# Optimization experiments

Hardware: AMD Instinct MI355X
Metric: run time of the kernel (lower is better)

The kernel has to match this reference:

```python
import jax, jax.numpy as jnp
import numpy as np

EPS = 1e-5  # torch InstanceNorm1d default eps
H = 64      # band_features


def instance_norm(x):
    # x: [B, T, F]; torch applies InstanceNorm1d on [B, F, T], i.e. normalize
    # over the length axis T per (batch, channel). No affine params.
    mu = jnp.mean(x, axis=1, keepdims=True)
    var = jnp.var(x, axis=1, keepdims=True)  # biased variance, as torch
    return (x - mu) * jax.lax.rsqrt(var + EPS)


def lstm_layer(x, Wih, Whh, bih, bhh):
    # x: [B, T, D_in]; Wih: [4H, D_in]; Whh: [4H, H]; gate order i,f,g,o (torch)
    B, T, _ = x.shape
    xp = jnp.einsum('btd,gd->btg', x, Wih) + bih + bhh   # [B, T, 4H]
    xp = jnp.swapaxes(xp, 0, 1)                          # [T, B, 4H]

    def step(carry, xt):
        h, c = carry
        gates = xt + h @ Whh.T                           # [B, 4H]
        i, f, g, o = jnp.split(gates, 4, axis=-1)
        c = jax.nn.sigmoid(f) * c + jax.nn.sigmoid(i) * jnp.tanh(g)
        h = jax.nn.sigmoid(o) * jnp.tanh(c)
        return (h, c), h

    h0 = jnp.zeros((B, H), x.dtype)
    _, hs = jax.lax.scan(step, (h0, h0), xp)             # hs: [T, B, H]
    return jnp.swapaxes(hs, 0, 1)                        # [B, T, H]


def setup_inputs() -> dict:
    key = jax.random.key(0)
    ks = jax.random.split(key, 12)
    B, T = 64, 4096
    bound = 1.0 / np.sqrt(H)  # torch LSTM/Linear default init scale

    def u(k, shape):
        return jax.random.uniform(k, shape, jnp.float32, -bound, bound)

    return {
        'x': jax.random.normal(ks[0], (B, T, H), jnp.float32),
        'Wih0': u(ks[1], (4 * H, H)), 'Whh0': u(ks[2], (4 * H, H)),
        'bih0': u(ks[3], (4 * H,)),   'bhh0': u(ks[4], (4 * H,)),
        'Wih1': u(ks[5], (4 * H, H)), 'Whh1': u(ks[6], (4 * H, H)),
        'bih1': u(ks[7], (4 * H,)),   'bhh1': u(ks[8], (4 * H,)),
        'Wfc': u(ks[9], (H, H)),      'bfc': u(ks[10], (H,)),
    }


def reference(x, Wih0, Whh0, bih0, bhh0, Wih1, Whh1, bih1, bhh1, Wfc, bfc):
    out = instance_norm(x)
    out = lstm_layer(out, Wih0, Whh0, bih0, bhh0)
    out = lstm_layer(out, Wih1, Whh1, bih1, bhh1)
    out = jnp.einsum('bth,oh->bto', out, Wfc) + bfc
    return out + x
```

## Files before the change

kernel.cpp:

```cpp
#include <hip/hip_runtime.h>
#include <hip/hip_bf16.h>
#include <cstddef>
#include <cstdint>

#define BB 64
#define TT 4096
#define HD 64
#define CH 16

__device__ __forceinline__ float sigf(float v) {
    return 1.0f / (1.0f + __expf(-v));
}
__device__ __forceinline__ float tanhf_fast(float v) {
    return 1.0f - 2.0f / (__expf(2.0f * v) + 1.0f);
}

__global__ __launch_bounds__(256) void stats_part(const float* __restrict__ x,
                                                  float* __restrict__ part) {
    const int b = blockIdx.x >> 2, seg = blockIdx.x & 3;
    const int f = threadIdx.x & 63, grp = threadIdx.x >> 6;
    const float* xb = x + (size_t)b * TT * HD + (size_t)seg * (TT / 4) * HD;
    float s = 0.f, s2 = 0.f;
    for (int t = grp; t < TT / 4; t += 4) {
        float v = xb[t * HD + f];
        s += v;
        s2 = fmaf(v, v, s2);
    }
    __shared__ float ls[4][64];
    __shared__ float ls2[4][64];
    ls[grp][f] = s;
    ls2[grp][f] = s2;
    __syncthreads();
    if (threadIdx.x < 64) {
        float ss = 0.f, ss2 = 0.f;
#pragma unroll
        for (int i = 0; i < 4; ++i) { ss += ls[i][f]; ss2 += ls2[i][f]; }
        part[blockIdx.x * HD + f] = ss;
        part[256 * HD + blockIdx.x * HD + f] = ss2;
    }
}

__global__ __launch_bounds__(64) void stats_fin(const float* __restrict__ part,
                                                float* __restrict__ stats) {
    const int b = blockIdx.x, f = threadIdx.x;
    float s = 0.f, s2 = 0.f;
#pragma unroll
    for (int seg = 0; seg < 4; ++seg) {
        s += part[(b * 4 + seg) * HD + f];
        s2 += part[256 * HD + (b * 4 + seg) * HD + f];
    }
    float mu = s * (1.0f / TT);
    float var = s2 * (1.0f / TT) - mu * mu;
    stats[b * HD + f] = mu;
    stats[BB * HD + b * HD + f] = rsqrtf(var + 1e-5f);
}

__global__ __launch_bounds__(512, 2) void rnn_fused(
    const float* __restrict__ x,
    const float* __restrict__ Wih0, const float* __restrict__ Whh0,
    const float* __restrict__ bih0, const float* __restrict__ bhh0,
    const float* __restrict__ Wih1, const float* __restrict__ Whh1,
    const float* __restrict__ bih1, const float* __restrict__ bhh1,
    const float* __restrict__ stats,
    float* __restrict__ h1out) {
    const int b = blockIdx.x;
    const int tid = threadIdx.x;
    const int g = tid >> 1;
    const int half = tid & 1;
    const int koff = half << 5;
    const int gtype = g >> 6;

    float4 wih0[8], whh0[8], wih1[8], whh1[8];
    {
        const float4* p0 = (const float4*)(Wih0 + g * HD + koff);
        const float4* p1 = (const float4*)(Whh0 + g * HD + koff);
        const float4* p2 = (const float4*)(Wih1 + g * HD + koff);
        const float4* p3 = (const float4*)(Whh1 + g * HD + koff);
#pragma unroll
        for (int r = 0; r < 8; ++r) {
            wih0[r] = p0[r];
            whh0[r] = p1[r];
            wih1[r] = p2[r];
            whh1[r] = p3[r];
        }
    }
    const float B0 = bih0[g] + bhh0[g];
    const float B1 = bih1[g] + bhh1[g];

    const int f0 = (2 * tid) & 63;
    const float mu0 = stats[b * HD + f0];
    const float mu1 = stats[b * HD + f0 + 1];
    const float rs0 = stats[BB * HD + b * HD + f0];
    const float rs1 = stats[BB * HD + b * HD + f0 + 1];

    __shared__ __align__(16) float h0_lds[HD];
    __shared__ __align__(16) float h1_lds[HD];
    __shared__ __align__(16) float gates_lds[512];
    __shared__ __align__(16) float xn[2][CH][HD];
    __shared__ __align__(16) float h1hist[CH][HD];

    const float* xrow = x + (size_t)b * TT * HD;
    float* hrow = h1out + (size_t)b * TT * HD;

    float c0 = 0.f, c1 = 0.f;

    {
        float2 v = ((const float2*)xrow)[tid];
        ((float2*)&xn[0][0][0])[tid] = make_float2((v.x - mu0) * rs0, (v.y - mu1) * rs1);
        if (tid < HD) { h0_lds[tid] = 0.f; h1_lds[tid] = 0.f; }
    }
    __syncthreads();
    {
        float q0 = 0.f, q1 = 0.f, q2 = 0.f, q3 = 0.f;
        const float4* xp = (const float4*)&xn[0][0][koff];
#pragma unroll
        for (int r = 0; r < 8; ++r) {
            float4 xq = xp[r];
            q0 = fmaf(wih0[r].x, xq.x, q0);
            q1 = fmaf(wih0[r].y, xq.y, q1);
            q2 = fmaf(wih0[r].z, xq.z, q2);
            q3 = fmaf(wih0[r].w, xq.w, q3);
        }
        float gp = (q0 + q1) + (q2 + q3);
        gp += __shfl_xor(gp, 1);
        gp += B0;
        float av = (gtype == 2) ? tanhf_fast(gp) : sigf(gp);
        if (half == 0) gates_lds[256 + g] = av;
    }
    __syncthreads();
    if (tid < HD) {
        float i0 = gates_lds[256 + tid], ff0 = gates_lds[320 + tid];
        float gg0 = gates_lds[384 + tid], o0 = gates_lds[448 + tid];
        c0 = i0 * gg0;
        h0_lds[tid] = o0 * tanhf_fast(c0);
        (void)ff0;
    }
    __syncthreads();

    float2 xs = make_float2(0.f, 0.f);
    for (int t = 0; t < TT; ++t) {
        const int tc = t & (CH - 1);

        if (tc == 0 && t + CH < TT) {
            xs = ((const float2*)(xrow + (size_t)(t + CH) * HD))[tid];
        }
        if (tc == (CH / 2) && t + CH / 2 < TT) {
            const int par = ((t >> 4) + 1) & 1;
            ((float2*)&xn[par][0][0])[tid] =
                make_float2((xs.x - mu0) * rs0, (xs.y - mu1) * rs1);
        }

        const int s1 = t + 1;
        const float4* h0p = (const float4*)&h0_lds[koff];
        const float4* h1p = (const float4*)&h1_lds[koff];
        const float4* xp = (const float4*)&xn[(s1 >> 4) & 1][s1 & (CH - 1)][koff];
        float a0 = 0.f, a1 = 0.f, a2 = 0.f, a3 = 0.f;
        float q0 = 0.f, q1 = 0.f, q2 = 0.f, q3 = 0.f;
#pragma unroll
        for (int r = 0; r < 8; ++r) {
            float4 h0q = h0p[r];
            float4 h1q = h1p[r];
            float4 xq = xp[r];
            a0 = fmaf(wih1[r].x, h0q.x, a0);
            a1 = fmaf(wih1[r].y, h0q.y, a1);
            a2 = fmaf(wih1[r].z, h0q.z, a2);
            a3 = fmaf(wih1[r].w, h0q.w, a3);
            a0 = fmaf(whh1[r].x, h1q.x, a0);
            a1 = fmaf(whh1[r].y, h1q.y, a1);
            a2 = fmaf(whh1[r].z, h1q.z, a2);
            a3 = fmaf(whh1[r].w, h1q.w, a3);
            q0 = fmaf(whh0[r].x, h0q.x, q0);
            q1 = fmaf(whh0[r].y, h0q.y, q1);
            q2 = fmaf(whh0[r].z, h0q.z, q2);
            q3 = fmaf(whh0[r].w, h0q.w, q3);
            q0 = fmaf(wih0[r].x, xq.x, q0);
            q1 = fmaf(wih0[r].y, xq.y, q1);
            q2 = fmaf(wih0[r].z, xq.z, q2);
            q3 = fmaf(wih0[r].w, xq.w, q3);
        }
        float g1 = (a0 + a1) + (a2 + a3);
        float g0v = (q0 + q1) + (q2 + q3);
        g1 += __shfl_xor(g1, 1);
        g0v += __shfl_xor(g0v, 1);
        g1 += B1;
        g0v += B0;
        float av1 = (gtype == 2) ? tanhf_fast(g1) : sigf(g1);
        float av0 = (gtype == 2) ? tanhf_fast(g0v) : sigf(g0v);
        if (half == 0) {
            gates_lds[g] = av1;
            gates_lds[256 + g] = av0;
        }
        __syncthreads();

        if (tid < HD) {
            float i1 = gates_lds[tid], f1 = gates_lds[64 + tid];
            float gg1 = gates_lds[128 + tid], o1 = gates_lds[192 + tid];
            float i0 = gates_lds[256 + tid], ff0 = gates_lds[320 + tid];
            float gg0 = gates_lds[384 + tid], o0 = gates_lds[448 + tid];
            c1 = fmaf(f1, c1, i1 * gg1);
            float hv1 = o1 * tanhf_fast(c1);
            h1_lds[tid] = hv1;
            h1hist[tc][tid] = hv1;
            c0 = fmaf(ff0, c0, i0 * gg0);
            h0_lds[tid] = o0 * tanhf_fast(c0);
        }
        __syncthreads();

        if (tc == CH - 1) {
            float2 hv = ((const float2*)&h1hist[0][0])[tid];
            ((float2*)(hrow + (size_t)(t - (CH - 1)) * HD))[tid] = hv;
        }
    }
}

__global__ __launch_bounds__(256) void fc_res(float* __restrict__ hout,
                                              const float* __restrict__ x,
                                              const float* __restrict__ Wfc,
                                              const float* __restrict__ bfc) {
    __shared__ __align__(16) float wfc_lds[HD * HD];
    __shared__ float bfc_lds[HD];
    const int tid = threadIdx.x;
#pragma unroll
    for (int i = 0; i < 4; ++i)
        ((float4*)wfc_lds)[tid + 256 * i] = ((const float4*)Wfc)[tid + 256 * i];
    if (tid < HD) bfc_lds[tid] = bfc[tid];

    const size_t row = (size_t)blockIdx.x * 256 + tid;
    float hr[HD];
    {
        const float4* hp = (const float4*)(hout + row * HD);
#pragma unroll
        for (int i = 0; i < 16; ++i) {
            float4 v = hp[i];
            hr[4 * i] = v.x; hr[4 * i + 1] = v.y;
            hr[4 * i + 2] = v.z; hr[4 * i + 3] = v.w;
        }
    }
    __syncthreads();

    const float4* xp = (const float4*)(x + row * HD);
    float4* op = (float4*)(hout + row * HD);
    for (int j4 = 0; j4 < 16; ++j4) {
        float s0 = 0.f, s1 = 0.f, s2 = 0.f, s3 = 0.f;
        const float* w0 = &wfc_lds[(4 * j4 + 0) * HD];
        const float* w1 = &wfc_lds[(4 * j4 + 1) * HD];
        const float* w2 = &wfc_lds[(4 * j4 + 2) * HD];
        const float* w3 = &wfc_lds[(4 * j4 + 3) * HD];
#pragma unroll
        for (int k = 0; k < HD; ++k) {
            s0 = fmaf(w0[k], hr[k], s0);
            s1 = fmaf(w1[k], hr[k], s1);
            s2 = fmaf(w2[k], hr[k], s2);
            s3 = fmaf(w3[k], hr[k], s3);
        }
        float4 xv = xp[j4];
        float4 o;
        o.x = s0 + bfc_lds[4 * j4 + 0] + xv.x;
        o.y = s1 + bfc_lds[4 * j4 + 1] + xv.y;
        o.z = s2 + bfc_lds[4 * j4 + 2] + xv.z;
        o.w = s3 + bfc_lds[4 * j4 + 3] + xv.w;
        op[j4] = o;
    }
}

extern "C" void kernel_launch(void* const* d_in, const int* in_sizes, int n_in,
                              void* d_out, int out_size, void* d_ws, size_t ws_size,
                              hipStream_t stream) {
    const float* x    = (const float*)d_in[0];
    const float* Wih0 = (const float*)d_in[1];
    const float* Whh0 = (const float*)d_in[2];
    const float* bih0 = (const float*)d_in[3];
    const float* bhh0 = (const float*)d_in[4];
    const float* Wih1 = (const float*)d_in[5];
    const float* Whh1 = (const float*)d_in[6];
    const float* bih1 = (const float*)d_in[7];
    const float* bhh1 = (const float*)d_in[8];
    const float* Wfc  = (const float*)d_in[9];
    const float* bfc  = (const float*)d_in[10];

    float* part  = (float*)d_ws;
    float* stats = part + 2 * 256 * HD;
    float* out   = (float*)d_out;

    stats_part<<<256, 256, 0, stream>>>(x, part);
    stats_fin<<<64, 64, 0, stream>>>(part, stats);
    rnn_fused<<<64, 512, 0, stream>>>(x, Wih0, Whh0, bih0, bhh0,
                                      Wih1, Whh1, bih1, bhh1, stats, out);
    fc_res<<<1024, 256, 0, stream>>>(out, x, Wfc, bfc);
}
```

Before: 3.934 ms.

## Repartition LSTM gate matvec across 8-lane groups with packed FMA and shuffle reduction

After: 3.554 ms. 9.7% less time.

```diff
diff --git a/kernel.cpp b/kernel.cpp
--- a/kernel.cpp
+++ b/kernel.cpp
@@ -1,12 +1,13 @@
 #include <hip/hip_runtime.h>
-#include <hip/hip_bf16.h>
 #include <cstddef>
 #include <cstdint>
 
 #define BB 64
 #define TT 4096
 #define HD 64
-#define CH 16
+#define CH 32
+
+typedef float v2f __attribute__((ext_vector_type(2)));
 
 __device__ __forceinline__ float sigf(float v) {
     return 1.0f / (1.0f + __expf(-v));
@@ -55,6 +56,54 @@
     stats[BB * HD + b * HD + f] = rsqrtf(var + 1e-5f);
 }
 
+__device__ __forceinline__ float gate8(const float* __restrict__ wa,
+                                       const float* __restrict__ wb,
+                                       const float* __restrict__ srcA,
+                                       const float* __restrict__ srcB,
+                                       int q) {
+    v2f sa[4], sb[4];
+    const v2f* pa = (const v2f*)(srcA + 8 * q);
+    const v2f* pb = (const v2f*)(srcB + 8 * q);
+#pragma unroll
+    for (int j = 0; j < 4; ++j) { sa[j] = pa[j]; sb[j] = pb[j]; }
+    float v[8];
+#pragma unroll
+    for (int r = 0; r < 8; ++r) {
+        v2f a;
+        a.x = 0.f; a.y = 0.f;
+#pragma unroll
+        for (int j = 0; j < 4; ++j) {
+            v2f wva, wvb;
+            wva.x = wa[r * 8 + 2 * j]; wva.y = wa[r * 8 + 2 * j + 1];
+            wvb.x = wb[r * 8 + 2 * j]; wvb.y = wb[r * 8 + 2 * j + 1];
+            a = __builtin_elementwise_fma(wva, sa[j], a);
+            a = __builtin_elementwise_fma(wvb, sb[j], a);
+        }
+        v[r] = a.x + a.y;
+    }
+    const bool b0 = q & 1, b1 = q & 2, b2 = q & 4;
+    float w0, w1, w2, w3;
+    {
+        float s0 = b0 ? v[0] : v[1], k0 = b0 ? v[1] : v[0];
+        float s1 = b0 ? v[2] : v[3], k1 = b0 ? v[3] : v[2];
+        float s2 = b0 ? v[4] : v[5], k2 = b0 ? v[5] : v[4];
+        float s3 = b0 ? v[6] : v[7], k3 = b0 ? v[7] : v[6];
+        w0 = k0 + __shfl_xor(s0, 1);
+        w1 = k1 + __shfl_xor(s1, 1);
+        w2 = k2 + __shfl_xor(s2, 1);
+        w3 = k3 + __shfl_xor(s3, 1);
+    }
+    float y0, y1;
+    {
+        float s0 = b1 ? w0 : w1, k0 = b1 ? w1 : w0;
+        float s1 = b1 ? w2 : w3, k1 = b1 ? w3 : w2;
+        y0 = k0 + __shfl_xor(s0, 2);
+        y1 = k1 + __shfl_xor(s1, 2);
+    }
+    float s0 = b2 ? y0 : y1, k0 = b2 ? y1 : y0;
+    return k0 + __shfl_xor(s0, 4);
+}
+
 __global__ __launch_bounds__(512, 2) void rnn_fused(
     const float* __restrict__ x,
     const float* __restrict__ Wih0, const float* __restrict__ Whh0,
@@ -65,37 +114,45 @@
     float* __restrict__ h1out) {
     const int b = blockIdx.x;
     const int tid = threadIdx.x;
-    const int g = tid >> 1;
-    const int half = tid & 1;
-    const int koff = half << 5;
-    const int gtype = g >> 6;
-
-    float4 wih0[8], whh0[8], wih1[8], whh1[8];
-    {
-        const float4* p0 = (const float4*)(Wih0 + g * HD + koff);
-        const float4* p1 = (const float4*)(Whh0 + g * HD + koff);
-        const float4* p2 = (const float4*)(Wih1 + g * HD + koff);
-        const float4* p3 = (const float4*)(Whh1 + g * HD + koff);
-#pragma unroll
-        for (int r = 0; r < 8; ++r) {
-            wih0[r] = p0[r];
-            whh0[r] = p1[r];
-            wih1[r] = p2[r];
-            whh1[r] = p3[r];
-        }
-    }
-    const float B0 = bih0[g] + bhh0[g];
-    const float B1 = bih1[g] + bhh1[g];
-
-    const int f0 = (2 * tid) & 63;
-    const float mu0 = stats[b * HD + f0];
-    const float mu1 = stats[b * HD + f0 + 1];
-    const float rs0 = stats[BB * HD + b * HD + f0];
-    const float rs1 = stats[BB * HD + b * HD + f0 + 1];
+    const int q = tid & 7;
+    const int rg = tid >> 3;
+    const bool isL1 = rg < 32;
+    const int r8 = (rg & 31) * 8;
+    const int gt = (tid >> 6) & 3;
+
+    const float* Wa = isL1 ? Wih1 : Whh0;
+    const float* Wb = isL1 ? Whh1 : Wih0;
+    float wa[64], wb[64];
+#pragma unroll
+    for (int r = 0; r < 8; ++r) {
+        const float4* pa = (const float4*)(Wa + (r8 + r) * HD + 8 * q);
+        const float4* pb = (const float4*)(Wb + (r8 + r) * HD + 8 * q);
+        float4 a0 = pa[0], a1 = pa[1];
+        float4 c0v = pb[0], c1v = pb[1];
+        wa[r * 8 + 0] = a0.x; wa[r * 8 + 1] = a0.y; wa[r * 8 + 2] = a0.z; wa[r * 8 + 3] = a0.w;
+        wa[r * 8 + 4] = a1.x; wa[r * 8 + 5] = a1.y; wa[r * 8 + 6] = a1.z; wa[r * 8 + 7] = a1.w;
+        wb[r * 8 + 0] = c0v.x; wb[r * 8 + 1] = c0v.y; wb[r * 8 + 2] = c0v.z; wb[r * 8 + 3] = c0v.w;
+        wb[r * 8 + 4] = c1v.x; wb[r * 8 + 5] = c1v.y; wb[r * 8 + 6] = c1v.z; wb[r * 8 + 7] = c1v.w;
+    }
+#pragma unroll
+    for (int i = 0; i < 64; ++i) {
+        asm volatile("" : "+v"(wa[i]), "+v"(wb[i]));
+    }
+
+    const int myrow = r8 + q;
+    const float Bsum = isL1 ? (bih1[myrow] + bhh1[myrow])
+                            : (bih0[myrow] + bhh0[myrow]);
+    const int feat = myrow & 63;
+    const int uu_w = feat ^ ((feat >> 3) & 7);
+    const int gofs = (isL1 ? 0 : 256) + 4 * uu_w + gt;
+
+    const int fb = (4 * tid) & 63;
+    const float4 mu4 = *(const float4*)&stats[b * HD + fb];
+    const float4 rs4 = *(const float4*)&stats[BB * HD + b * HD + fb];
 
     __shared__ __align__(16) float h0_lds[HD];
     __shared__ __align__(16) float h1_lds[HD];
-    __shared__ __align__(16) float gates_lds[512];
+    __shared__ __align__(16) float glds[512];
     __shared__ __align__(16) float xn[2][CH][HD];
     __shared__ __align__(16) float h1hist[CH][HD];
 
@@ -104,111 +161,74 @@
 
     float c0 = 0.f, c1 = 0.f;
 
-    {
-        float2 v = ((const float2*)xrow)[tid];
-        ((float2*)&xn[0][0][0])[tid] = make_float2((v.x - mu0) * rs0, (v.y - mu1) * rs1);
-        if (tid < HD) { h0_lds[tid] = 0.f; h1_lds[tid] = 0.f; }
-    }
-    __syncthreads();
-    {
-        float q0 = 0.f, q1 = 0.f, q2 = 0.f, q3 = 0.f;
-        const float4* xp = (const float4*)&xn[0][0][koff];
-#pragma unroll
-        for (int r = 0; r < 8; ++r) {
-            float4 xq = xp[r];
-            q0 = fmaf(wih0[r].x, xq.x, q0);
-            q1 = fmaf(wih0[r].y, xq.y, q1);
-            q2 = fmaf(wih0[r].z, xq.z, q2);
-            q3 = fmaf(wih0[r].w, xq.w, q3);
-        }
-        float gp = (q0 + q1) + (q2 + q3);
-        gp += __shfl_xor(gp, 1);
-        gp += B0;
-        float av = (gtype == 2) ? tanhf_fast(gp) : sigf(gp);
-        if (half == 0) gates_lds[256 + g] = av;
+    if (tid < HD) { h0_lds[tid] = 0.f; h1_lds[tid] = 0.f; }
+    {
+        float4 xv = ((const float4*)xrow)[tid];
+        float4 xnv;
+        xnv.x = (xv.x - mu4.x) * rs4.x;
+        xnv.y = (xv.y - mu4.y) * rs4.y;
+        xnv.z = (xv.z - mu4.z) * rs4.z;
+        xnv.w = (xv.w - mu4.w) * rs4.w;
+        ((float4*)&xn[0][0][0])[tid] = xnv;
+    }
+    __syncthreads();
+    {
+        const float* srcB = isL1 ? h1_lds : &xn[0][0][0];
+        float gpre = gate8(wa, wb, h0_lds, srcB, q) + Bsum;
+        float av = (gt == 2) ? tanhf_fast(gpre) : sigf(gpre);
+        glds[gofs] = av;
     }
     __syncthreads();
     if (tid < HD) {
-        float i0 = gates_lds[256 + tid], ff0 = gates_lds[320 + tid];
-        float gg0 = gates_lds[384 + tid], o0 = gates_lds[448 + tid];
-        c0 = i0 * gg0;
-        h0_lds[tid] = o0 * tanhf_fast(c0);
-        (void)ff0;
-    }
-    __syncthreads();
-
-    float2 xs = make_float2(0.f, 0.f);
+        const int f = tid;
+        const int uu = f ^ ((f >> 3) & 7);
+        float4 G0 = *(const float4*)&glds[256 + 4 * uu];
+        c0 = G0.x * G0.z;
+        h0_lds[f] = G0.w * tanhf_fast(c0);
+    }
+    __syncthreads();
+
+    float4 xs = make_float4(0.f, 0.f, 0.f, 0.f);
     for (int t = 0; t < TT; ++t) {
         const int tc = t & (CH - 1);
 
         if (tc == 0 && t + CH < TT) {
-            xs = ((const float2*)(xrow + (size_t)(t + CH) * HD))[tid];
-        }
-        if (tc == (CH / 2) && t + CH / 2 < TT) {
-            const int par = ((t >> 4) + 1) & 1;
-            ((float2*)&xn[par][0][0])[tid] =
-                make_float2((xs.x - mu0) * rs0, (xs.y - mu1) * rs1);
+            xs = ((const float4*)(xrow + (size_t)(t + CH) * HD))[tid];
+        }
+        if (tc == CH / 2 && t + CH / 2 < TT) {
+            const int pn = ((t >> 5) + 1) & 1;
+            float4 xnv;
+            xnv.x = (xs.x - mu4.x) * rs4.x;
+            xnv.y = (xs.y - mu4.y) * rs4.y;
+            xnv.z = (xs.z - mu4.z) * rs4.z;
+            xnv.w = (xs.w - mu4.w) * rs4.w;
+            ((float4*)&xn[pn][0][0])[tid] = xnv;
         }
 
         const int s1 = t + 1;
-        const float4* h0p = (const float4*)&h0_lds[koff];
-        const float4* h1p = (const float4*)&h1_lds[koff];
-        const float4* xp = (const float4*)&xn[(s1 >> 4) & 1][s1 & (CH - 1)][koff];
-        float a0 = 0.f, a1 = 0.f, a2 = 0.f, a3 = 0.f;
-        float q0 = 0.f, q1 = 0.f, q2 = 0.f, q3 = 0.f;
-#pragma unroll
-        for (int r = 0; r < 8; ++r) {
-            float4 h0q = h0p[r];
-            float4 h1q = h1p[r];
-            float4 xq = xp[r];
-            a0 = fmaf(wih1[r].x, h0q.x, a0);
-            a1 = fmaf(wih1[r].y, h0q.y, a1);
-            a2 = fmaf(wih1[r].z, h0q.z, a2);
-            a3 = fmaf(wih1[r].w, h0q.w, a3);
-            a0 = fmaf(whh1[r].x, h1q.x, a0);
-            a1 = fmaf(whh1[r].y, h1q.y, a1);
-            a2 = fmaf(whh1[r].z, h1q.z, a2);
-            a3 = fmaf(whh1[r].w, h1q.w, a3);
-            q0 = fmaf(whh0[r].x, h0q.x, q0);
-            q1 = fmaf(whh0[r].y, h0q.y, q1);
-            q2 = fmaf(whh0[r].z, h0q.z, q2);
-            q3 = fmaf(whh0[r].w, h0q.w, q3);
-            q0 = fmaf(wih0[r].x, xq.x, q0);
-            q1 = fmaf(wih0[r].y, xq.y, q1);
-            q2 = fmaf(wih0[r].z, xq.z, q2);
-            q3 = fmaf(wih0[r].w, xq.w, q3);
-        }
-        float g1 = (a0 + a1) + (a2 + a3);
-        float g0v = (q0 + q1) + (q2 + q3);
-        g1 += __shfl_xor(g1, 1);
-        g0v += __shfl_xor(g0v, 1);
-        g1 += B1;
-        g0v += B0;
-        float av1 = (gtype == 2) ? tanhf_fast(g1) : sigf(g1);
-        float av0 = (gtype == 2) ? tanhf_fast(g0v) : sigf(g0v);
-        if (half == 0) {
-            gates_lds[g] = av1;
-            gates_lds[256 + g] = av0;
-        }
+        const float* srcB = isL1 ? h1_lds : &xn[(s1 >> 5) & 1][s1 & (CH - 1)][0];
+        float gpre = gate8(wa, wb, h0_lds, srcB, q) + Bsum;
+        float av = (gt == 2) ? tanhf_fast(gpre) : sigf(gpre);
+        glds[gofs] = av;
         __syncthreads();
 
         if (tid < HD) {
-            float i1 = gates_lds[tid], f1 = gates_lds[64 + tid];
-            float gg1 = gates_lds[128 + tid], o1 = gates_lds[192 + tid];
-            float i0 = gates_lds[256 + tid], ff0 = gates_lds[320 + tid];
-            float gg0 = gates_lds[384 + tid], o0 = gates_lds[448 + tid];
-            c1 = fmaf(f1, c1, i1 * gg1);
-            float hv1 = o1 * tanhf_fast(c1);
-            h1_lds[tid] = hv1;
-            h1hist[tc][tid] = hv1;
-            c0 = fmaf(ff0, c0, i0 * gg0);
-            h0_lds[tid] = o0 * tanhf_fast(c0);
+            const int f = tid;
+            const int uu = f ^ ((f >> 3) & 7);
+            float4 G1 = *(const float4*)&glds[4 * uu];
+            float4 G0 = *(const float4*)&glds[256 + 4 * uu];
+            c1 = fmaf(G1.y, c1, G1.x * G1.z);
+            float hv1 = G1.w * tanhf_fast(c1);
+            h1_lds[f] = hv1;
+            h1hist[tc][f] = hv1;
+            c0 = fmaf(G0.y, c0, G0.x * G0.z);
+            h0_lds[f] = G0.w * tanhf_fast(c0);
         }
         __syncthreads();
 
         if (tc == CH - 1) {
-            float2 hv = ((const float2*)&h1hist[0][0])[tid];
-            ((float2*)(hrow + (size_t)(t - (CH - 1)) * HD))[tid] = hv;
+            float4 hv = ((const float4*)&h1hist[0][0])[tid];
+            ((float4*)(hrow + (size_t)(t - (CH - 1)) * HD))[tid] = hv;
         }
     }
 }
```

## Batch 16 sequences per block and compute LSTM gates with fp16 MFMA

Applied to the files above, without the earlier changes.

Result: slower. 6.549 ms (+66.5%).

```diff
diff --git a/kernel.cpp b/kernel.cpp
--- a/kernel.cpp
+++ b/kernel.cpp
@@ -1,19 +1,19 @@
 #include <hip/hip_runtime.h>
-#include <hip/hip_bf16.h>
 #include <cstddef>
 #include <cstdint>
 
 #define BB 64
 #define TT 4096
 #define HD 64
-#define CH 16
-
-__device__ __forceinline__ float sigf(float v) {
-    return 1.0f / (1.0f + __expf(-v));
-}
-__device__ __forceinline__ float tanhf_fast(float v) {
-    return 1.0f - 2.0f / (__expf(2.0f * v) + 1.0f);
-}
+#define FP 72
+
+typedef _Float16 f16;
+typedef _Float16 f16x8 __attribute__((ext_vector_type(8)));
+typedef _Float16 f16x4 __attribute__((ext_vector_type(4)));
+typedef float f32x4 __attribute__((ext_vector_type(4)));
+
+__device__ __forceinline__ float sigf(float v) { return 1.0f / (1.0f + __expf(-v)); }
+__device__ __forceinline__ float tanhf_fast(float v) { return 1.0f - 2.0f / (__expf(2.0f * v) + 1.0f); }
 
 __global__ __launch_bounds__(256) void stats_part(const float* __restrict__ x,
                                                   float* __restrict__ part) {
@@ -55,7 +55,7 @@
     stats[BB * HD + b * HD + f] = rsqrtf(var + 1e-5f);
 }
 
-__global__ __launch_bounds__(512, 2) void rnn_fused(
+__global__ __launch_bounds__(512, 2) void rnn_mfma(
     const float* __restrict__ x,
     const float* __restrict__ Wih0, const float* __restrict__ Whh0,
     const float* __restrict__ bih0, const float* __restrict__ bhh0,
@@ -63,153 +63,148 @@
     const float* __restrict__ bih1, const float* __restrict__ bhh1,
     const float* __restrict__ stats,
     float* __restrict__ h1out) {
-    const int b = blockIdx.x;
+    const int blk = blockIdx.x;
     const int tid = threadIdx.x;
-    const int g = tid >> 1;
-    const int half = tid & 1;
-    const int koff = half << 5;
-    const int gtype = g >> 6;
-
-    float4 wih0[8], whh0[8], wih1[8], whh1[8];
-    {
-        const float4* p0 = (const float4*)(Wih0 + g * HD + koff);
-        const float4* p1 = (const float4*)(Whh0 + g * HD + koff);
-        const float4* p2 = (const float4*)(Wih1 + g * HD + koff);
-        const float4* p3 = (const float4*)(Whh1 + g * HD + koff);
-#pragma unroll
-        for (int r = 0; r < 8; ++r) {
-            wih0[r] = p0[r];
-            whh0[r] = p1[r];
-            wih1[r] = p2[r];
-            whh1[r] = p3[r];
-        }
-    }
-    const float B0 = bih0[g] + bhh0[g];
-    const float B1 = bih1[g] + bhh1[g];
-
-    const int f0 = (2 * tid) & 63;
-    const float mu0 = stats[b * HD + f0];
-    const float mu1 = stats[b * HD + f0 + 1];
-    const float rs0 = stats[BB * HD + b * HD + f0];
-    const float rs1 = stats[BB * HD + b * HD + f0 + 1];
-
-    __shared__ __align__(16) float h0_lds[HD];
-    __shared__ __align__(16) float h1_lds[HD];
-    __shared__ __align__(16) float gates_lds[512];
-    __shared__ __align__(16) float xn[2][CH][HD];
-    __shared__ __align__(16) float h1hist[CH][HD];
-
-    const float* xrow = x + (size_t)b * TT * HD;
-    float* hrow = h1out + (size_t)b * TT * HD;
-
-    float c0 = 0.f, c1 = 0.f;
-
-    {
-        float2 v = ((const float2*)xrow)[tid];
-        ((float2*)&xn[0][0][0])[tid] = make_float2((v.x - mu0) * rs0, (v.y - mu1) * rs1);
-        if (tid < HD) { h0_lds[tid] = 0.f; h1_lds[tid] = 0.f; }
-    }
-    __syncthreads();
-    {
-        float q0 = 0.f, q1 = 0.f, q2 = 0.f, q3 = 0.f;
-        const float4* xp = (const float4*)&xn[0][0][koff];
-#pragma unroll
-        for (int r = 0; r < 8; ++r) {
-            float4 xq = xp[r];
-            q0 = fmaf(wih0[r].x, xq.x, q0);
-            q1 = fmaf(wih0[r].y, xq.y, q1);
-            q2 = fmaf(wih0[r].z, xq.z, q2);
-            q3 = fmaf(wih0[r].w, xq.w, q3);
-        }
-        float gp = (q0 + q1) + (q2 + q3);
-        gp += __shfl_xor(gp, 1);
-        gp += B0;
-        float av = (gtype == 2) ? tanhf_fast(gp) : sigf(gp);
-        if (half == 0) gates_lds[256 + g] = av;
-    }
-    __syncthreads();
-    if (tid < HD) {
-        float i0 = gates_lds[256 + tid], ff0 = gates_lds[320 + tid];
-        float gg0 = gates_lds[384 + tid], o0 = gates_lds[448 + tid];
-        c0 = i0 * gg0;
-        h0_lds[tid] = o0 * tanhf_fast(c0);
-        (void)ff0;
-    }
-    __syncthreads();
-
-    float2 xs = make_float2(0.f, 0.f);
+    const int lane = tid & 63;
+    const int wid = tid >> 6;
+    const bool L1w = (wid < 4);
+    const int wq = L1w ? wid : (wid - 4);
+    const int ln15 = lane & 15;
+    const int l16 = lane >> 4;
+
+    __shared__ __align__(16) f16 hT0[2][16 * FP];
+    __shared__ __align__(16) f16 hT1[16][16 * FP];
+    __shared__ __align__(16) f16 xnb[2][8][16 * FP];
+
+    const float* WA = L1w ? Wih1 : Whh0;
+    const float* WBm = L1w ? Whh1 : Wih0;
+    f16x8 wA[4][2], wB[4][2];
+#pragma unroll
+    for (int i = 0; i < 4; ++i) {
+        const int row = 16 * (wq + 4 * i) + ln15;
+#pragma unroll
+        for (int kt = 0; kt < 2; ++kt) {
+            const int fb = 32 * kt + 8 * l16;
+            const float4 a0 = *(const float4*)&WA[row * HD + fb];
+            const float4 a1 = *(const float4*)&WA[row * HD + fb + 4];
+            const float4 b0 = *(const float4*)&WBm[row * HD + fb];
+            const float4 b1 = *(const float4*)&WBm[row * HD + fb + 4];
+            wA[i][kt] = (f16x8){(f16)a0.x, (f16)a0.y, (f16)a0.z, (f16)a0.w,
+                                (f16)a1.x, (f16)a1.y, (f16)a1.z, (f16)a1.w};
+            wB[i][kt] = (f16x8){(f16)b0.x, (f16)b0.y, (f16)b0.z, (f16)b0.w,
+                                (f16)b1.x, (f16)b1.y, (f16)b1.z, (f16)b1.w};
+        }
+    }
+
+    const int phi = 16 * wq + ln15;
+    const float* bi = L1w ? bih1 : bih0;
+    const float* bh = L1w ? bhh1 : bhh0;
+    float bias[4];
+#pragma unroll
+    for (int i = 0; i < 4; ++i) bias[i] = bi[64 * i + phi] + bh[64 * i + phi];
+
+    const int sb = tid >> 5;
+    const int sq = (tid >> 1) & 15;
+    const int sth = tid & 1;
+    const size_t gb = (size_t)blk * 16 + sb;
+    const float4 mu4 = *(const float4*)&stats[gb * HD + 4 * sq];
+    const float4 rs4 = *(const float4*)&stats[(size_t)BB * HD + gb * HD + 4 * sq];
+    const float* xrow = x + gb * TT * HD;
+    float* orow = h1out + gb * TT * HD;
+
+    for (int i = tid; i < 2 * 16 * FP / 2; i += 512) ((unsigned*)hT0)[i] = 0u;
+    for (int i = tid; i < 16 * 16 * FP / 2; i += 512) ((unsigned*)hT1)[i] = 0u;
+
+#pragma unroll
+    for (int i = 0; i < 4; ++i) {
+        const int tau = sth * 4 + i;
+        float4 v = *(const float4*)&xrow[(size_t)tau * HD + 4 * sq];
+        f16x4 h4 = {(f16)((v.x - mu4.x) * rs4.x), (f16)((v.y - mu4.y) * rs4.y),
+                    (f16)((v.z - mu4.z) * rs4.z), (f16)((v.w - mu4.w) * rs4.w)};
+        *(f16x4*)&xnb[0][tau][sb * FP + 4 * sq] = h4;
+    }
+
+    float cst[4] = {0.f, 0.f, 0.f, 0.f};
+
+    auto PHASE = [&](int t) {
+        f16x8 A0[2], A1[2];
+        {
+            const f16* base = &hT0[t & 1][ln15 * FP + 8 * l16];
+            A0[0] = *(const f16x8*)(base);
+            A0[1] = *(const f16x8*)(base + 32);
+        }
+        {
+            const f16* bb2 = L1w ? &hT1[(t + 15) & 15][0]
+                                 : &xnb[((t + 1) >> 3) & 1][(t + 1) & 7][0];
+            const f16* base = bb2 + ln15 * FP + 8 * l16;
+            A1[0] = *(const f16x8*)(base);
+            A1[1] = *(const f16x8*)(base + 32);
+        }
+        f32x4 acc[4];
+#pragma unroll
+        for (int i = 0; i < 4; ++i) {
+            acc[i] = (f32x4){0.f, 0.f, 0.f, 0.f};
+            acc[i] = __builtin_amdgcn_mfma_f32_16x16x32_f16(A0[0], wA[i][0], acc[i], 0, 0, 0);
+            acc[i] = __builtin_amdgcn_mfma_f32_16x16x32_f16(A0[1], wA[i][1], acc[i], 0, 0, 0);
+            acc[i] = __builtin_amdgcn_mfma_f32_16x16x32_f16(A1[0], wB[i][0], acc[i], 0, 0, 0);
+            acc[i] = __builtin_amdgcn_mfma_f32_16x16x32_f16(A1[1], wB[i][1], acc[i], 0, 0, 0);
+        }
+        f16* dest = L1w ? &hT1[t & 15][0] : &hT0[(t + 1) & 1][0];
+#pragma unroll
+        for (int r = 0; r < 4; ++r) {
+            float ai = sigf(acc[0][r] + bias[0]);
+            float af = sigf(acc[1][r] + bias[1]);
+            float ag = tanhf_fast(acc[2][r] + bias[2]);
+            float ao = sigf(acc[3][r] + bias[3]);
+            float c = fmaf(af, cst[r], ai * ag);
+            cst[r] = c;
+            float h = ao * tanhf_fast(c);
+            dest[(4 * l16 + r) * FP + phi] = (f16)h;
+        }
+    };
+
+    __syncthreads();
+    if (!L1w) PHASE(-1);
+    __syncthreads();
+
+    float4 xr[4];
     for (int t = 0; t < TT; ++t) {
-        const int tc = t & (CH - 1);
-
-        if (tc == 0 && t + CH < TT) {
-            xs = ((const float2*)(xrow + (size_t)(t + CH) * HD))[tid];
-        }
-        if (tc == (CH / 2) && t + CH / 2 < TT) {
-            const int par = ((t >> 4) + 1) & 1;
-            ((float2*)&xn[par][0][0])[tid] =
-                make_float2((xs.x - mu0) * rs0, (xs.y - mu1) * rs1);
-        }
-
-        const int s1 = t + 1;
-        const float4* h0p = (const float4*)&h0_lds[koff];
-        const float4* h1p = (const float4*)&h1_lds[koff];
-        const float4* xp = (const float4*)&xn[(s1 >> 4) & 1][s1 & (CH - 1)][koff];
-        float a0 = 0.f, a1 = 0.f, a2 = 0.f, a3 = 0.f;
-        float q0 = 0.f, q1 = 0.f, q2 = 0.f, q3 = 0.f;
-#pragma unroll
-        for (int r = 0; r < 8; ++r) {
-            float4 h0q = h0p[r];
-            float4 h1q = h1p[r];
-            float4 xq = xp[r];
-            a0 = fmaf(wih1[r].x, h0q.x, a0);
-            a1 = fmaf(wih1[r].y, h0q.y, a1);
-            a2 = fmaf(wih1[r].z, h0q.z, a2);
-            a3 = fmaf(wih1[r].w, h0q.w, a3);
-            a0 = fmaf(whh1[r].x, h1q.x, a0);
-            a1 = fmaf(whh1[r].y, h1q.y, a1);
-            a2 = fmaf(whh1[r].z, h1q.z, a2);
-            a3 = fmaf(whh1[r].w, h1q.w, a3);
-            q0 = fmaf(whh0[r].x, h0q.x, q0);
-            q1 = fmaf(whh0[r].y, h0q.y, q1);
-            q2 = fmaf(whh0[r].z, h0q.z, q2);
-            q3 = fmaf(whh0[r].w, h0q.w, q3);
-            q0 = fmaf(wih0[r].x, xq.x, q0);
-            q1 = fmaf(wih0[r].y, xq.y, q1);
-            q2 = fmaf(wih0[r].z, xq.z, q2);
-            q3 = fmaf(wih0[r].w, xq.w, q3);
-        }
-        float g1 = (a0 + a1) + (a2 + a3);
-        float g0v = (q0 + q1) + (q2 + q3);
-        g1 += __shfl_xor(g1, 1);
-        g0v += __shfl_xor(g0v, 1);
-        g1 += B1;
-        g0v += B0;
-        float av1 = (gtype == 2) ? tanhf_fast(g1) : sigf(g1);
-        float av0 = (gtype == 2) ? tanhf_fast(g0v) : sigf(g0v);
-        if (half == 0) {
-            gates_lds[g] = av1;
-            gates_lds[256 + g] = av0;
+        const int tc = t & 7;
+        const int cn = (t >> 3) + 1;
+        if (tc == 0 && cn < 512) {
+#pragma unroll
+            for (int i = 0; i < 4; ++i)
+                xr[i] = *(const float4*)&xrow[(size_t)(cn * 8 + sth * 4 + i) * HD + 4 * sq];
+        }
+        PHASE(t);
+        if (tc == 5 && cn < 512) {
+#pragma unroll
+            for (int i = 0; i < 4; ++i) {
+                const int tau = sth * 4 + i;
+                f16x4 h4 = {(f16)((xr[i].x - mu4.x) * rs4.x), (f16)((xr[i].y - mu4.y) * rs4.y),
+                            (f16)((xr[i].z - mu4.z) * rs4.z), (f16)((xr[i].w - mu4.w) * rs4.w)};
+                *(f16x4*)&xnb[cn & 1][tau][sb * FP + 4 * sq] = h4;
+            }
+        }
+        if (tc == 3 && t >= 11) {
+            const int fch = (t >> 3) - 1;
+            const int sbase = (fch & 1) * 8;
+#pragma unroll
+            for (int i = 0; i < 4; ++i) {
+                const int tau = sth * 4 + i;
+                f16x4 hv = *(const f16x4*)&hT1[sbase + tau][sb * FP + 4 * sq];
+                float4 o = {(float)hv[0], (float)hv[1], (float)hv[2], (float)hv[3]};
+                *(float4*)&orow[(size_t)(fch * 8 + tau) * HD + 4 * sq] = o;
+            }
         }
         __syncthreads();
-
-        if (tid < HD) {
-            float i1 = gates_lds[tid], f1 = gates_lds[64 + tid];
-            float gg1 = gates_lds[128 + tid], o1 = gates_lds[192 + tid];
-            float i0 = gates_lds[256 + tid], ff0 = gates_lds[320 + tid];
-            float gg0 = gates_lds[384 + tid], o0 = gates_lds[448 + tid];
-            c1 = fmaf(f1, c1, i1 * gg1);
-            float hv1 = o1 * tanhf_fast(c1);
-            h1_lds[tid] = hv1;
-            h1hist[tc][tid] = hv1;
-            c0 = fmaf(ff0, c0, i0 * gg0);
-            h0_lds[tid] = o0 * tanhf_fast(c0);
-        }
-        __syncthreads();
-
-        if (tc == CH - 1) {
-            float2 hv = ((const float2*)&h1hist[0][0])[tid];
-            ((float2*)(hrow + (size_t)(t - (CH - 1)) * HD))[tid] = hv;
-        }
+    }
+#pragma unroll
+    for (int i = 0; i < 4; ++i) {
+        const int tau = sth * 4 + i;
+        f16x4 hv = *(const f16x4*)&hT1[8 + tau][sb * FP + 4 * sq];
+        float4 o = {(float)hv[0], (float)hv[1], (float)hv[2], (float)hv[3]};
+        *(float4*)&orow[(size_t)(511 * 8 + tau) * HD + 4 * sq] = o;
     }
 }
 
@@ -284,7 +279,7 @@
 
     stats_part<<<256, 256, 0, stream>>>(x, part);
     stats_fin<<<64, 64, 0, stream>>>(part, stats);
-    rnn_fused<<<64, 512, 0, stream>>>(x, Wih0, Whh0, bih0, bhh0,
-                                      Wih1, Whh1, bih1, bhh1, stats, out);
+    rnn_mfma<<<4, 512, 0, stream>>>(x, Wih0, Whh0, bih0, bhh0,
+                                    Wih1, Whh1, bih1, bhh1, stats, out);
     fc_res<<<1024, 256, 0, stream>>>(out, x, Wfc, bfc);
 }
```
